# Performance work log

Hardware: AMD Instinct MI355X
Metric: run time of the kernel (lower is better)

The kernel has to match this reference:

```python
import jax, jax.numpy as jnp
import numpy as np

N, D, FF, NH = 500000, 128, 256, 4
GRIDS = [0.5, 1.0, 2.0]


def setup_inputs() -> dict:
    key = jax.random.key(0)
    ks = jax.random.split(key, 8)
    h = jax.random.normal(ks[0], (N, D), jnp.float32)
    coords = jax.random.uniform(ks[1], (N, 3), jnp.float32) * 8.0
    c = np.asarray(coords)
    invs, Ms = [], []
    for g in GRIDS:
        vox = np.floor(c / g).astype(np.int64)
        _, inv = np.unique(vox, axis=0, return_inverse=True)
        invs.append(jnp.asarray(inv.reshape(-1).astype(np.int32)))
        Ms.append(int(inv.max()) + 1)
    S = len(GRIDS)
    sc = 0.02
    def rn(k, shape):
        return jax.random.normal(k, shape, jnp.float32) * sc
    params = dict(
        Wqkv=rn(ks[2], (S, 3 * D, D)), bqkv=jnp.zeros((S, 3 * D), jnp.float32),
        Wo=rn(ks[3], (S, D, D)), bo=jnp.zeros((S, D), jnp.float32),
        ln1_s=jnp.ones((S, D), jnp.float32), ln1_b=jnp.zeros((S, D), jnp.float32),
        W1=rn(ks[4], (S, FF, D)), b1=jnp.zeros((S, FF), jnp.float32),
        W2=rn(ks[5], (S, D, FF)), b2=jnp.zeros((S, D), jnp.float32),
        ln2_s=jnp.ones((S, D), jnp.float32), ln2_b=jnp.zeros((S, D), jnp.float32),
        Wf=rn(ks[6], (D, D * (S + 1))), bf=jnp.zeros((D,), jnp.float32),
    )
    return dict(h=h, coords=coords, inv0=invs[0], inv1=invs[1], inv2=invs[2],
                M0=Ms[0], M1=Ms[1], M2=Ms[2], **params)


def _ln(x, s, b):
    m = x.mean(-1, keepdims=True)
    v = ((x - m) ** 2).mean(-1, keepdims=True)
    return (x - m) * jax.lax.rsqrt(v + 1e-5) * s + b


def _forward(h, invs, Ms, Wqkv, bqkv, Wo, bo, ln1_s, ln1_b, W1, b1, W2, b2, ln2_s, ln2_b, Wf, bf):
    dh = D // NH
    feats = [h]
    for i, (inv, M) in enumerate(zip(invs, Ms)):
        # scatter-mean pooling into M voxels (counts clamped >= 1)
        macro = jax.ops.segment_sum(h, inv, num_segments=M)  # [M, D]
        counts = jax.ops.segment_sum(jnp.ones((h.shape[0], 1), h.dtype), inv, num_segments=M)
        macro = macro / jnp.maximum(counts, 1.0)
        # TransformerEncoderLayer (post-norm, relu), batch of 1 -> drop batch dim
        qkv = macro @ Wqkv[i].T + bqkv[i]
        q, k, v = (t.reshape(M, NH, dh) for t in jnp.split(qkv, 3, axis=-1))
        scores = jnp.einsum('mhd,nhd->hmn', q, k) / jnp.sqrt(jnp.float32(dh))
        attn = jax.nn.softmax(scores, axis=-1)
        o = jnp.einsum('hmn,nhd->mhd', attn, v).reshape(M, D) @ Wo[i].T + bo[i]
        x = _ln(macro + o, ln1_s[i], ln1_b[i])
        ffo = jax.nn.relu(x @ W1[i].T + b1[i]) @ W2[i].T + b2[i]
        x = _ln(x + ffo, ln2_s[i], ln2_b[i])
        feats.append(x[inv])  # broadcast gather back to particles [N, D]
    return jnp.concatenate(feats, axis=-1) @ Wf.T + bf


def reference(h, coords, inv0, inv1, inv2, M0, M1, M2, Wqkv, bqkv, Wo, bo, ln1_s, ln1_b, W1, b1, W2, b2, ln2_s, ln2_b, Wf, bf):
    return _forward(h, (inv0, inv1, inv2), (M0, M1, M2), Wqkv, bqkv, Wo, bo,
                    ln1_s, ln1_b, W1, b1, W2, b2, ln2_s, ln2_b, Wf, bf)
```

## Files before the change

kernel.cpp:

```cpp
#include <hip/hip_runtime.h>
#include <hip/hip_bf16.h>

#define MC 4096
#define DD 128
#define NHH 4
#define DH 32
#define FFD 256
#define NS 3
#define NSPLIT 4
#define PLEN 1024

typedef __attribute__((ext_vector_type(8))) short short8_t;
typedef __attribute__((ext_vector_type(4))) float f32x4;

__device__ __forceinline__ int getM(int s, const int* M0, const int* M1, const int* M2) {
    return (s == 0) ? *M0 : (s == 1) ? *M1 : *M2;
}

__device__ __forceinline__ unsigned short f2bf(float f) {
    unsigned int u = __float_as_uint(f);
    u += 0x7FFFu + ((u >> 16) & 1u);
    return (unsigned short)(u >> 16);
}

__device__ __forceinline__ short8_t pack8(float4 a, float4 b) {
    short8_t r;
    r[0] = (short)f2bf(a.x); r[1] = (short)f2bf(a.y);
    r[2] = (short)f2bf(a.z); r[3] = (short)f2bf(a.w);
    r[4] = (short)f2bf(b.x); r[5] = (short)f2bf(b.y);
    r[6] = (short)f2bf(b.z); r[7] = (short)f2bf(b.w);
    return r;
}

__device__ __forceinline__ f32x4 max4(f32x4 a, f32x4 b) {
    f32x4 r;
    r[0] = fmaxf(a[0], b[0]); r[1] = fmaxf(a[1], b[1]);
    r[2] = fmaxf(a[2], b[2]); r[3] = fmaxf(a[3], b[3]);
    return r;
}
__device__ __forceinline__ f32x4 shflx4(f32x4 a, int m) {
    f32x4 r;
    r[0] = __shfl_xor(a[0], m); r[1] = __shfl_xor(a[1], m);
    r[2] = __shfl_xor(a[2], m); r[3] = __shfl_xor(a[3], m);
    return r;
}
__device__ __forceinline__ f32x4 exp4(f32x4 a) {
    f32x4 r;
    r[0] = __expf(a[0]); r[1] = __expf(a[1]);
    r[2] = __expf(a[2]); r[3] = __expf(a[3]);
    return r;
}

__global__ void k_parent(const int* __restrict__ inv0, const int* __restrict__ inv1,
                         const int* __restrict__ inv2,
                         int* __restrict__ parent10, int* __restrict__ parent21,
                         int* __restrict__ cnt, int N)
{
    int n = blockIdx.x * blockDim.x + threadIdx.x;
    if (n >= N) return;
    int i0 = inv0[n];
    parent10[i0] = inv1[n];
    parent21[inv1[n]] = inv2[n];
    atomicAdd(&cnt[i0], 1);
}

__global__ void k_scan(const int* __restrict__ cnt, int* __restrict__ offs)
{
    __shared__ int arr[1024];
    int tid = threadIdx.x;
    int base = tid * 4;
    int c0 = cnt[base], c1 = cnt[base + 1], c2 = cnt[base + 2], c3 = cnt[base + 3];
    int tot = c0 + c1 + c2 + c3;
    arr[tid] = tot;
    __syncthreads();
    for (int off = 1; off < 1024; off <<= 1) {
        int v = (tid >= off) ? arr[tid - off] : 0;
        __syncthreads();
        arr[tid] += v;
        __syncthreads();
    }
    int excl = arr[tid] - tot;
    offs[base] = excl;
    offs[base + 1] = excl + c0;
    offs[base + 2] = excl + c0 + c1;
    offs[base + 3] = excl + c0 + c1 + c2;
}

__global__ void k_place(const int* __restrict__ inv0, const int* __restrict__ offs,
                        int* __restrict__ fill, int* __restrict__ order, int N)
{
    int n = blockIdx.x * blockDim.x + threadIdx.x;
    if (n >= N) return;
    int i0 = inv0[n];
    int pos = offs[i0] + atomicAdd(&fill[i0], 1);
    order[pos] = n;
}

__global__ __launch_bounds__(256) void k_pool(const float* __restrict__ h,
                                              const int* __restrict__ order,
                                              const int* __restrict__ offs,
                                              const int* __restrict__ cnt,
                                              float* __restrict__ sum0, float* __restrict__ cnt0,
                                              const int* __restrict__ M0)
{
    int v = blockIdx.x;
    if (v >= *M0) return;
    int beg = offs[v], len = cnt[v];
    int tid = threadIdx.x;
    int dg = tid & 31;
    int rs = tid >> 5;
    const int* op = order + beg;

    float ax = 0.f, ay = 0.f, az = 0.f, aw = 0.f;
    int j = rs;
    for (; j + 8 < len; j += 16) {
        int r0 = op[j];
        int r1 = op[j + 8];
        float4 a = *(const float4*)(h + (size_t)r0 * DD + dg * 4);
        float4 b = *(const float4*)(h + (size_t)r1 * DD + dg * 4);
        ax += a.x + b.x; ay += a.y + b.y; az += a.z + b.z; aw += a.w + b.w;
    }
    if (j < len) {
        int r0 = op[j];
        float4 a = *(const float4*)(h + (size_t)r0 * DD + dg * 4);
        ax += a.x; ay += a.y; az += a.z; aw += a.w;
    }

    __shared__ __align__(16) float red[8][DD];
    *(float4*)&red[rs][dg * 4] = make_float4(ax, ay, az, aw);
    __syncthreads();
    if (tid < 32) {
        float4 t0 = *(const float4*)&red[0][tid * 4];
        float4 t1 = *(const float4*)&red[1][tid * 4];
        float4 t2 = *(const float4*)&red[2][tid * 4];
        float4 t3 = *(const float4*)&red[3][tid * 4];
        float4 t4 = *(const float4*)&red[4][tid * 4];
        float4 t5 = *(const float4*)&red[5][tid * 4];
        float4 t6 = *(const float4*)&red[6][tid * 4];
        float4 t7 = *(const float4*)&red[7][tid * 4];
        float4 r;
        r.x = ((t0.x + t1.x) + (t2.x + t3.x)) + ((t4.x + t5.x) + (t6.x + t7.x));
        r.y = ((t0.y + t1.y) + (t2.y + t3.y)) + ((t4.y + t5.y) + (t6.y + t7.y));
        r.z = ((t0.z + t1.z) + (t2.z + t3.z)) + ((t4.z + t5.z) + (t6.z + t7.z));
        r.w = ((t0.w + t1.w) + (t2.w + t3.w)) + ((t4.w + t5.w) + (t6.w + t7.w));
        *(float4*)(sum0 + (size_t)v * DD + tid * 4) = r;
        if (tid == 0) cnt0[v] = (float)len;
    }
}

__global__ void k_rollup(const float* __restrict__ sumSrc, const float* __restrict__ cntSrc,
                         const int* __restrict__ parent,
                         float* __restrict__ sumDst, float* __restrict__ cntDst,
                         const int* __restrict__ Msrc, int cap)
{
    int idx = blockIdx.x * blockDim.x + threadIdx.x;
    int v = idx >> 7, d = idx & 127;
    int Ms = *Msrc;
    if (Ms > cap) Ms = cap;
    if (v >= Ms) return;
    int p = parent[v];
    atomicAdd(&sumDst[(size_t)p * DD + d], sumSrc[idx]);
    if (d == 0) atomicAdd(&cntDst[p], cntSrc[v]);
}

__global__ void k_finalize(float* __restrict__ macro, const float* __restrict__ counts,
                           const int* M0, const int* M1, const int* M2)
{
    int idx = blockIdx.x * blockDim.x + threadIdx.x;
    int s = idx / (MC * DD);
    int r = (idx >> 7) & (MC - 1);
    if (r >= getM(s, M0, M1, M2)) return;
    float c = counts[s * MC + r];
    macro[idx] /= fmaxf(c, 1.0f);
}

__global__ void k_b0frag(const float* __restrict__ Wf, unsigned short* __restrict__ b0f)
{
    int idx = blockIdx.x * 256 + threadIdx.x;
    int j = idx & 7, l = (idx >> 3) & 63, kt = (idx >> 9) & 3, nt = idx >> 11;
    int d = nt * 16 + (l & 15);
    int k = kt * 32 + (l >> 4) * 8 + j;
    b0f[idx] = f2bf(Wf[(size_t)d * (4 * DD) + k]);
}

__global__ void k_qkv(const float* __restrict__ macro, const float* __restrict__ Wqkv,
                      const float* __restrict__ bqkv, float* __restrict__ qkv,
                      const int* M0, const int* M1, const int* M2)
{
    int s = blockIdx.y;
    int Ms = getM(s, M0, M1, M2);
    int row0 = blockIdx.x * 8;
    if (row0 >= Ms) return;
    __shared__ __align__(16) float mac[8][DD];
    int tid = threadIdx.x;
    for (int e = tid; e < 8 * DD; e += 256) {
        int r = e >> 7, d = e & 127;
        int row = row0 + r;
        mac[r][d] = (row < Ms) ? macro[(size_t)s * MC * DD + (size_t)row * DD + d] : 0.0f;
    }
    __syncthreads();
    for (int j = tid; j < 3 * DD; j += 256) {
        const float* w = Wqkv + ((size_t)s * 3 * DD + j) * DD;
        float b = bqkv[s * 3 * DD + j];
        float acc[8];
#pragma unroll
        for (int r = 0; r < 8; ++r) acc[r] = b;
        for (int k = 0; k < DD; k += 4) {
            float4 w4 = *(const float4*)(w + k);
#pragma unroll
            for (int r = 0; r < 8; ++r) {
                float4 m4 = *(const float4*)&mac[r][k];
                acc[r] += w4.x * m4.x + w4.y * m4.y + w4.z * m4.z + w4.w * m4.w;
            }
        }
        for (int r = 0; r < 8; ++r) {
            int row = row0 + r;
            if (row < Ms) qkv[((size_t)s * MC + row) * (3 * DD) + j] = acc[r];
        }
    }
}

__global__ __launch_bounds__(256) void k_attn_part(const float* __restrict__ qkv,
                                                   float* __restrict__ part_o,
                                                   float* __restrict__ part_ml,
                                                   const int* M0, const int* M1, const int* M2)
{
    int z = blockIdx.z;
    int s = z / NSPLIT, part = z % NSPLIT;
    int head = blockIdx.y;
    int Ms = getM(s, M0, M1, M2);
    int q0 = blockIdx.x * 64;
    if (q0 >= Ms) return;
    int kstart = part * PLEN;
    if (kstart >= Ms) return;
    int kend = kstart + PLEN; if (kend > Ms) kend = Ms;

    __shared__ __align__(16) unsigned short kf[4][64][8];
    __shared__ __align__(16) unsigned short vf[2][2][64][8];
    __shared__ __align__(16) unsigned short pf[4][16][80];

    int tid = threadIdx.x;
    int wave = tid >> 6, lane = tid & 63;
    int c = lane & 15, g = lane >> 4;

    const float* base = qkv + (size_t)s * MC * 3 * DD;
    const float* Qb = base + head * DH;
    const float* Kb = base + DD + head * DH;
    const float* Vb = base + 2 * DD + head * DH;

    short8_t qfrag = {0,0,0,0,0,0,0,0};
    {
        int qr = q0 + wave * 16 + c;
        if (qr < Ms) {
            const float* qp = Qb + (size_t)qr * 3 * DD + g * 8;
            qfrag = pack8(*(const float4*)qp, *(const float4*)(qp + 4));
        }
    }

    f32x4 o0 = {0.f, 0.f, 0.f, 0.f}, o1 = {0.f, 0.f, 0.f, 0.f};
    f32x4 mreg = {-1e30f, -1e30f, -1e30f, -1e30f};
    f32x4 lreg = {0.f, 0.f, 0.f, 0.f};
    const float scale = 0.1767766952966369f;

    int sko = tid >> 2, sg = tid & 3;
    int s_nt = sko >> 4;
    int s_l  = (sko & 15) | (sg << 4);
    int s_ks = sko >> 5, s_kk = sko & 31;
    int s_j  = s_kk & 7, s_hi = (s_kk >> 3) & 3;
    int s_vnt = sg >> 1, s_db = (sg & 1) * 8;

    for (int kb = kstart; kb < kend; kb += 64) {
        __syncthreads();
        {
            int key = kb + sko;
            short8_t kv = {0,0,0,0,0,0,0,0};
            if (key < kend) {
                const float* kr = Kb + (size_t)key * 3 * DD + sg * 8;
                kv = pack8(*(const float4*)kr, *(const float4*)(kr + 4));
            }
            *(short8_t*)&kf[s_nt][s_l][0] = kv;
        }
        {
            int key = kb + sko;
            float4 a = make_float4(0.f, 0.f, 0.f, 0.f);
            float4 b = make_float4(0.f, 0.f, 0.f, 0.f);
            if (key < kend) {
                const float* vr = Vb + (size_t)key * 3 * DD + sg * 8;
                a = *(const float4*)vr;
                b = *(const float4*)(vr + 4);
            }
            unsigned short* vslot = &vf[s_ks][s_vnt][0][0];
            vslot[((s_db + 0) | (s_hi << 4)) * 8 + s_j] = f2bf(a.x);
            vslot[((s_db + 1) | (s_hi << 4)) * 8 + s_j] = f2bf(a.y);
            vslot[((s_db + 2) | (s_hi << 4)) * 8 + s_j] = f2bf(a.z);
            vslot[((s_db + 3) | (s_hi << 4)) * 8 + s_j] = f2bf(a.w);
            vslot[((s_db + 4) | (s_hi << 4)) * 8 + s_j] = f2bf(b.x);
            vslot[((s_db + 5) | (s_hi << 4)) * 8 + s_j] = f2bf(b.y);
            vslot[((s_db + 6) | (s_hi << 4)) * 8 + s_j] = f2bf(b.z);
            vslot[((s_db + 7) | (s_hi << 4)) * 8 + s_j] = f2bf(b.w);
        }
        __syncthreads();

        f32x4 zero = {0.f, 0.f, 0.f, 0.f};
        short8_t kf0 = *(const short8_t*)&kf[0][lane][0];
        short8_t kf1 = *(const short8_t*)&kf[1][lane][0];
        short8_t kf2 = *(const short8_t*)&kf[2][lane][0];
        short8_t kf3 = *(const short8_t*)&kf[3][lane][0];
        f32x4 a0 = __builtin_amdgcn_mfma_f32_16x16x32_bf16(qfrag, kf0, zero, 0, 0, 0);
        f32x4 a1 = __builtin_amdgcn_mfma_f32_16x16x32_bf16(qfrag, kf1, zero, 0, 0, 0);
        f32x4 a2 = __builtin_amdgcn_mfma_f32_16x16x32_bf16(qfrag, kf2, zero, 0, 0, 0);
        f32x4 a3 = __builtin_amdgcn_mfma_f32_16x16x32_bf16(qfrag, kf3, zero, 0, 0, 0);

        f32x4 neg = {-1e30f, -1e30f, -1e30f, -1e30f};
        a0 = (kb +  0 + c < kend) ? a0 * scale : neg;
        a1 = (kb + 16 + c < kend) ? a1 * scale : neg;
        a2 = (kb + 32 + c < kend) ? a2 * scale : neg;
        a3 = (kb + 48 + c < kend) ? a3 * scale : neg;

        f32x4 rmax = max4(max4(a0, a1), max4(a2, a3));
        rmax = max4(rmax, shflx4(rmax, 1));
        rmax = max4(rmax, shflx4(rmax, 2));
        rmax = max4(rmax, shflx4(rmax, 4));
        rmax = max4(rmax, shflx4(rmax, 8));
        f32x4 mnew = max4(mreg, rmax);
        f32x4 alpha = exp4(mreg - mnew);
        mreg = mnew;
        lreg = lreg * alpha;
        o0 = o0 * alpha;
        o1 = o1 * alpha;

        a0 = exp4(a0 - mnew);
        a1 = exp4(a1 - mnew);
        a2 = exp4(a2 - mnew);
        a3 = exp4(a3 - mnew);
        f32x4 rsum = (a0 + a1) + (a2 + a3);
        rsum = rsum + shflx4(rsum, 1);
        rsum = rsum + shflx4(rsum, 2);
        rsum = rsum + shflx4(rsum, 4);
        rsum = rsum + shflx4(rsum, 8);
        lreg = lreg + rsum;

        {
            unsigned short* prow = &pf[wave][0][0];
            int rb = g * 4;
            prow[(rb + 0) * 80 +  0 + c] = f2bf(a0[0]);
            prow[(rb + 1) * 80 +  0 + c] = f2bf(a0[1]);
            prow[(rb + 2) * 80 +  0 + c] = f2bf(a0[2]);
            prow[(rb + 3) * 80 +  0 + c] = f2bf(a0[3]);
            prow[(rb + 0) * 80 + 16 + c] = f2bf(a1[0]);
            prow[(rb + 1) * 80 + 16 + c] = f2bf(a1[1]);
            prow[(rb + 2) * 80 + 16 + c] = f2bf(a1[2]);
            prow[(rb + 3) * 80 + 16 + c] = f2bf(a1[3]);
            prow[(rb + 0) * 80 + 32 + c] = f2bf(a2[0]);
            prow[(rb + 1) * 80 + 32 + c] = f2bf(a2[1]);
            prow[(rb + 2) * 80 + 32 + c] = f2bf(a2[2]);
            prow[(rb + 3) * 80 + 32 + c] = f2bf(a2[3]);
            prow[(rb + 0) * 80 + 48 + c] = f2bf(a3[0]);
            prow[(rb + 1) * 80 + 48 + c] = f2bf(a3[1]);
            prow[(rb + 2) * 80 + 48 + c] = f2bf(a3[2]);
            prow[(rb + 3) * 80 + 48 + c] = f2bf(a3[3]);
        }

        {
            short8_t p0 = *(const short8_t*)&pf[wave][c][ 0 + g * 8];
            short8_t v00 = *(const short8_t*)&vf[0][0][lane][0];
            short8_t v01 = *(const short8_t*)&vf[0][1][lane][0];
            o0 = __builtin_amdgcn_mfma_f32_16x16x32_bf16(p0, v00, o0, 0, 0, 0);
            o1 = __builtin_amdgcn_mfma_f32_16x16x32_bf16(p0, v01, o1, 0, 0, 0);
            short8_t p1 = *(const short8_t*)&pf[wave][c][32 + g * 8];
            short8_t v10 = *(const short8_t*)&vf[1][0][lane][0];
            short8_t v11 = *(const short8_t*)&vf[1][1][lane][0];
            o0 = __builtin_amdgcn_mfma_f32_16x16x32_bf16(p1, v10, o0, 0, 0, 0);
            o1 = __builtin_amdgcn_mfma_f32_16x16x32_bf16(p1, v11, o1, 0, 0, 0);
        }
    }

    int rec = ((s * NHH + head) * 64 + blockIdx.x) * NSPLIT + part;
    float* po = part_o + (size_t)rec * 2048;
    int qb = wave * 16 + g * 4;
    po[(qb + 0) * 32 + c] = o0[0];
    po[(qb + 1) * 32 + c] = o0[1];
    po[(qb + 2) * 32 + c] = o0[2];
    po[(qb + 3) * 32 + c] = o0[3];
    po[(qb + 0) * 32 + 16 + c] = o1[0];
    po[(qb + 1) * 32 + 16 + c] = o1[1];
    po[(qb + 2) * 32 + 16 + c] = o1[2];
    po[(qb + 3) * 32 + 16 + c] = o1[3];
    if (c == 0) {
        part_ml[rec * 128 + qb + 0] = mreg[0];
        part_ml[rec * 128 + qb + 1] = mreg[1];
        part_ml[rec * 128 + qb + 2] = mreg[2];
        part_ml[rec * 128 + qb + 3] = mreg[3];
        part_ml[rec * 128 + 64 + qb + 0] = lreg[0];
        part_ml[rec * 128 + 64 + qb + 1] = lreg[1];
        part_ml[rec * 128 + 64 + qb + 2] = lreg[2];
        part_ml[rec * 128 + 64 + qb + 3] = lreg[3];
    }
}

__global__ void k_attn_comb(const float* __restrict__ part_o, const float* __restrict__ part_ml,
                            float* __restrict__ attno,
                            const int* M0, const int* M1, const int* M2)
{
    int s = blockIdx.z, head = blockIdx.y;
    int Ms = getM(s, M0, M1, M2);
    int q0 = blockIdx.x * 64;
    if (q0 >= Ms) return;
    int tid = threadIdx.x;
    int qi = tid >> 2, sub = tid & 3;
    int nparts = (Ms + PLEN - 1) / PLEN;
    if (nparts > NSPLIT) nparts = NSPLIT;
    int recbase = ((s * NHH + head) * 64 + blockIdx.x) * NSPLIT;

    float m = -1e30f;
    for (int p = 0; p < nparts; ++p)
        m = fmaxf(m, part_ml[(recbase + p) * 128 + qi]);
    float L = 0.f;
    float4 A0 = {0,0,0,0}, A1 = {0,0,0,0};
    for (int p = 0; p < nparts; ++p) {
        float mp = part_ml[(recbase + p) * 128 + qi];
        float lp = part_ml[(recbase + p) * 128 + 64 + qi];
        float w = __expf(mp - m);
        L += lp * w;
        const float* po = part_o + (size_t)(recbase + p) * 2048;
        float4 a = *(const float4*)(po + qi * 32 + sub * 4);
        float4 b = *(const float4*)(po + qi * 32 + (sub + 4) * 4);
        A0.x += a.x * w; A0.y += a.y * w; A0.z += a.z * w; A0.w += a.w * w;
        A1.x += b.x * w; A1.y += b.y * w; A1.z += b.z * w; A1.w += b.w * w;
    }
    if (q0 + qi < Ms) {
        float inv = 1.0f / fmaxf(L, 1e-30f);
        size_t orow = ((size_t)s * MC + q0 + qi) * DD + head * DH;
        float4 r0 = make_float4(A0.x * inv, A0.y * inv, A0.z * inv, A0.w * inv);
        float4 r1 = make_float4(A1.x * inv, A1.y * inv, A1.z * inv, A1.w * inv);
        *(float4*)(attno + orow + sub * 4) = r0;
        *(float4*)(attno + orow + (sub + 4) * 4) = r1;
    }
}

__global__ __launch_bounds__(256) void k_layer(const float* __restrict__ macro,
                                               const float* __restrict__ attno,
                                               const float* __restrict__ Wo, const float* __restrict__ bo,
                                               const float* __restrict__ ln1s, const float* __restrict__ ln1b,
                                               const float* __restrict__ W1, const float* __restrict__ b1,
                                               const float* __restrict__ W2, const float* __restrict__ b2,
                                               const float* __restrict__ ln2s, const float* __restrict__ ln2b,
                                               const float* __restrict__ Wf,
                                               float* __restrict__ y,
                                               const int* M0, const int* M1, const int* M2)
{
    int s = blockIdx.y;
    int Ms = getM(s, M0, M1, M2);
    int row0 = blockIdx.x * 8;
    if (row0 >= Ms) return;
    __shared__ __align__(16) float os8[8][DD];
    __shared__ __align__(16) float xr8[8][DD];
    __shared__ __align__(16) float ts8[8][FFD];
    __shared__ float mv[8][2];
    int tid = threadIdx.x;
    int rr = tid >> 5, tt = tid & 31;

    {
        int row = row0 + rr;
        float4 v = make_float4(0.f, 0.f, 0.f, 0.f);
        if (row < Ms) v = *(const float4*)(attno + ((size_t)s * MC + row) * DD + tt * 4);
        *(float4*)&os8[rr][tt * 4] = v;
    }
    __syncthreads();

    float acc[8];

    if (tid < DD) {
        const float* w = Wo + ((size_t)s * DD + tid) * DD;
        float b = bo[s * DD + tid];
#pragma unroll
        for (int r = 0; r < 8; ++r) acc[r] = b;
        for (int k = 0; k < DD; k += 4) {
            float4 w4 = *(const float4*)(w + k);
#pragma unroll
            for (int r = 0; r < 8; ++r) {
                float4 m4 = *(const float4*)&os8[r][k];
                acc[r] += w4.x * m4.x + w4.y * m4.y + w4.z * m4.z + w4.w * m4.w;
            }
        }
#pragma unroll
        for (int r = 0; r < 8; ++r) {
            int row = row0 + r;
            float res = (row < Ms) ? macro[((size_t)s * MC + row) * DD + tid] : 0.f;
            xr8[r][tid] = acc[r] + res;
        }
    }
    __syncthreads();

    {
        float4 v = *(const float4*)&xr8[rr][tt * 4];
        float su = v.x + v.y + v.z + v.w;
        float sq = v.x * v.x + v.y * v.y + v.z * v.z + v.w * v.w;
        for (int off = 16; off >= 1; off >>= 1) { su += __shfl_xor(su, off); sq += __shfl_xor(sq, off); }
        if (tt == 0) { mv[rr][0] = su; mv[rr][1] = sq; }
    }
    __syncthreads();
    {
        float mean = mv[rr][0] * (1.0f / DD);
        float var = fmaxf(mv[rr][1] * (1.0f / DD) - mean * mean, 0.0f);
        float rstd = rsqrtf(var + 1e-5f);
        float4 v = *(const float4*)&xr8[rr][tt * 4];
        float4 gs = *(const float4*)(ln1s + s * DD + tt * 4);
        float4 gb = *(const float4*)(ln1b + s * DD + tt * 4);
        float4 o;
        o.x = (v.x - mean) * rstd * gs.x + gb.x;
        o.y = (v.y - mean) * rstd * gs.y + gb.y;
        o.z = (v.z - mean) * rstd * gs.z + gb.z;
        o.w = (v.w - mean) * rstd * gs.w + gb.w;
        *(float4*)&xr8[rr][tt * 4] = o;
    }
    __syncthreads();

    {
        const float* w = W1 + ((size_t)s * FFD + tid) * DD;
        float b = b1[s * FFD + tid];
#pragma unroll
        for (int r = 0; r < 8; ++r) acc[r] = b;
        for (int k = 0; k < DD; k += 4) {
            float4 w4 = *(const float4*)(w + k);
#pragma unroll
            for (int r = 0; r < 8; ++r) {
                float4 m4 = *(const float4*)&xr8[r][k];
                acc[r] += w4.x * m4.x + w4.y * m4.y + w4.z * m4.z + w4.w * m4.w;
            }
        }
#pragma unroll
        for (int r = 0; r < 8; ++r) ts8[r][tid] = fmaxf(acc[r], 0.0f);
    }
    __syncthreads();

    if (tid < DD) {
        const float* w = W2 + ((size_t)s * DD + tid) * FFD;
        float b = b2[s * DD + tid];
#pragma unroll
        for (int r = 0; r < 8; ++r) acc[r] = b;
        for (int k = 0; k < FFD; k += 4) {
            float4 w4 = *(const float4*)(w + k);
#pragma unroll
            for (int r = 0; r < 8; ++r) {
                float4 m4 = *(const float4*)&ts8[r][k];
                acc[r] += w4.x * m4.x + w4.y * m4.y + w4.z * m4.z + w4.w * m4.w;
            }
        }
#pragma unroll
        for (int r = 0; r < 8; ++r) os8[r][tid] = acc[r] + xr8[r][tid];
    }
    __syncthreads();

    {
        float4 v = *(const float4*)&os8[rr][tt * 4];
        float su = v.x + v.y + v.z + v.w;
        float sq = v.x * v.x + v.y * v.y + v.z * v.z + v.w * v.w;
        for (int off = 16; off >= 1; off >>= 1) { su += __shfl_xor(su, off); sq += __shfl_xor(sq, off); }
        if (tt == 0) { mv[rr][0] = su; mv[rr][1] = sq; }
    }
    __syncthreads();
    {
        float mean = mv[rr][0] * (1.0f / DD);
        float var = fmaxf(mv[rr][1] * (1.0f / DD) - mean * mean, 0.0f);
        float rstd = rsqrtf(var + 1e-5f);
        float4 v = *(const float4*)&os8[rr][tt * 4];
        float4 gs = *(const float4*)(ln2s + s * DD + tt * 4);
        float4 gb = *(const float4*)(ln2b + s * DD + tt * 4);
        float4 o;
        o.x = (v.x - mean) * rstd * gs.x + gb.x;
        o.y = (v.y - mean) * rstd * gs.y + gb.y;
        o.z = (v.z - mean) * rstd * gs.z + gb.z;
        o.w = (v.w - mean) * rstd * gs.w + gb.w;
        *(float4*)&os8[rr][tt * 4] = o;
    }
    __syncthreads();

    if (tid < DD) {
        const float* w = Wf + (size_t)tid * (4 * DD) + (s + 1) * DD;
#pragma unroll
        for (int r = 0; r < 8; ++r) acc[r] = 0.f;
        for (int k = 0; k < DD; k += 4) {
            float4 w4 = *(const float4*)(w + k);
#pragma unroll
            for (int r = 0; r < 8; ++r) {
                float4 m4 = *(const float4*)&os8[r][k];
                acc[r] += w4.x * m4.x + w4.y * m4.y + w4.z * m4.z + w4.w * m4.w;
            }
        }
#pragma unroll
        for (int r = 0; r < 8; ++r) {
            int row = row0 + r;
            if (row < Ms) y[((size_t)s * MC + row) * DD + tid] = acc[r];
        }
    }
}

__global__ void k_ycomb(const float* __restrict__ y, const int* __restrict__ parent10,
                        const int* __restrict__ parent21, const float* __restrict__ bf,
                        float* __restrict__ yc, const int* __restrict__ M0)
{
    int idx = blockIdx.x * 256 + threadIdx.x;
    int v = idx >> 7, d = idx & 127;
    if (v >= *M0) return;
    int p1 = parent10[v];
    int p2 = parent21[p1];
    yc[idx] = y[(size_t)v * DD + d] + y[((size_t)MC + p1) * DD + d]
            + y[((size_t)2 * MC + p2) * DD + d] + bf[d];
}

__global__ __launch_bounds__(256) void k_final(const float* __restrict__ h,
                                               const unsigned short* __restrict__ b0f,
                                               const float* __restrict__ yc,
                                               const int* __restrict__ inv0,
                                               float* __restrict__ out, int N)
{
    int tid = threadIdx.x;
    int wave = tid >> 6, lane = tid & 63;
    int c = lane & 15, g = lane >> 4;

    int ntasks = (N + 15) >> 4;
    int pair = blockIdx.x * 4 + wave;
    int taskA = pair * 2;
    if (taskA >= ntasks) return;
    int taskB = taskA + 1;

    int pA = taskA * 16 + c;
    int pB = taskB * 16 + c;
    bool okA = (pA < N);
    bool okB = (taskB < ntasks) && (pB < N);

    short8_t hA0 = {0,0,0,0,0,0,0,0}, hA1 = hA0, hA2 = hA0, hA3 = hA0;
    short8_t hB0 = hA0, hB1 = hA0, hB2 = hA0, hB3 = hA0;
    int iA = 0, iB = 0;
    if (okA) {
        const float* hr = h + (size_t)pA * DD + g * 8;
        hA0 = pack8(*(const float4*)(hr +  0), *(const float4*)(hr +  4));
        hA1 = pack8(*(const float4*)(hr + 32), *(const float4*)(hr + 36));
        hA2 = pack8(*(const float4*)(hr + 64), *(const float4*)(hr + 68));
        hA3 = pack8(*(const float4*)(hr + 96), *(const float4*)(hr + 100));
        iA = inv0[pA];
    }
    if (okB) {
        const float* hr = h + (size_t)pB * DD + g * 8;
        hB0 = pack8(*(const float4*)(hr +  0), *(const float4*)(hr +  4));
        hB1 = pack8(*(const float4*)(hr + 32), *(const float4*)(hr + 36));
        hB2 = pack8(*(const float4*)(hr + 64), *(const float4*)(hr + 68));
        hB3 = pack8(*(const float4*)(hr + 96), *(const float4*)(hr + 100));
        iB = inv0[pB];
    }
    const float* ycA = yc + (size_t)iA * DD;
    const float* ycB = yc + (size_t)iB * DD;

#pragma unroll
    for (int ntp = 0; ntp < 4; ++ntp) {
        int nt0 = ntp * 2, nt1 = ntp * 2 + 1;
        f32x4 aA0 = {0.f, 0.f, 0.f, 0.f}, aA1 = {0.f, 0.f, 0.f, 0.f};
        f32x4 aB0 = {0.f, 0.f, 0.f, 0.f}, aB1 = {0.f, 0.f, 0.f, 0.f};
        {
            short8_t w00 = *(const short8_t*)(b0f + (size_t)((nt0 * 4 + 0) * 64 + lane) * 8);
            aA0 = __builtin_amdgcn_mfma_f32_16x16x32_bf16(w00, hA0, aA0, 0, 0, 0);
            aB0 = __builtin_amdgcn_mfma_f32_16x16x32_bf16(w00, hB0, aB0, 0, 0, 0);
            short8_t w10 = *(const short8_t*)(b0f + (size_t)((nt1 * 4 + 0) * 64 + lane) * 8);
            aA1 = __builtin_amdgcn_mfma_f32_16x16x32_bf16(w10, hA0, aA1, 0, 0, 0);
            aB1 = __builtin_amdgcn_mfma_f32_16x16x32_bf16(w10, hB0, aB1, 0, 0, 0);
            short8_t w01 = *(const short8_t*)(b0f + (size_t)((nt0 * 4 + 1) * 64 + lane) * 8);
            aA0 = __builtin_amdgcn_mfma_f32_16x16x32_bf16(w01, hA1, aA0, 0, 0, 0);
            aB0 = __builtin_amdgcn_mfma_f32_16x16x32_bf16(w01, hB1, aB0, 0, 0, 0);
            short8_t w11 = *(const short8_t*)(b0f + (size_t)((nt1 * 4 + 1) * 64 + lane) * 8);
            aA1 = __builtin_amdgcn_mfma_f32_16x16x32_bf16(w11, hA1, aA1, 0, 0, 0);
            aB1 = __builtin_amdgcn_mfma_f32_16x16x32_bf16(w11, hB1, aB1, 0, 0, 0);
            short8_t w02 = *(const short8_t*)(b0f + (size_t)((nt0 * 4 + 2) * 64 + lane) * 8);
            aA0 = __builtin_amdgcn_mfma_f32_16x16x32_bf16(w02, hA2, aA0, 0, 0, 0);
            aB0 = __builtin_amdgcn_mfma_f32_16x16x32_bf16(w02, hB2, aB0, 0, 0, 0);
            short8_t w12 = *(const short8_t*)(b0f + (size_t)((nt1 * 4 + 2) * 64 + lane) * 8);
            aA1 = __builtin_amdgcn_mfma_f32_16x16x32_bf16(w12, hA2, aA1, 0, 0, 0);
            aB1 = __builtin_amdgcn_mfma_f32_16x16x32_bf16(w12, hB2, aB1, 0, 0, 0);
            short8_t w03 = *(const short8_t*)(b0f + (size_t)((nt0 * 4 + 3) * 64 + lane) * 8);
            aA0 = __builtin_amdgcn_mfma_f32_16x16x32_bf16(w03, hA3, aA0, 0, 0, 0);
            aB0 = __builtin_amdgcn_mfma_f32_16x16x32_bf16(w03, hB3, aB0, 0, 0, 0);
            short8_t w13 = *(const short8_t*)(b0f + (size_t)((nt1 * 4 + 3) * 64 + lane) * 8);
            aA1 = __builtin_amdgcn_mfma_f32_16x16x32_bf16(w13, hA3, aA1, 0, 0, 0);
            aB1 = __builtin_amdgcn_mfma_f32_16x16x32_bf16(w13, hB3, aB1, 0, 0, 0);
        }
        int d0 = nt0 * 16 + g * 4;
        int d1 = d0 + 16;
        if (okA) {
            float4 g0 = *(const float4*)(ycA + d0);
            float4 g1 = *(const float4*)(ycA + d1);
            float4 r0, r1;
            r0.x = aA0[0] + g0.x; r0.y = aA0[1] + g0.y; r0.z = aA0[2] + g0.z; r0.w = aA0[3] + g0.w;
            r1.x = aA1[0] + g1.x; r1.y = aA1[1] + g1.y; r1.z = aA1[2] + g1.z; r1.w = aA1[3] + g1.w;
            *(float4*)(out + (size_t)pA * DD + d0) = r0;
            *(float4*)(out + (size_t)pA * DD + d1) = r1;
        }
        if (okB) {
            float4 g0 = *(const float4*)(ycB + d0);
            float4 g1 = *(const float4*)(ycB + d1);
            float4 r0, r1;
            r0.x = aB0[0] + g0.x; r0.y = aB0[1] + g0.y; r0.z = aB0[2] + g0.z; r0.w = aB0[3] + g0.w;
            r1.x = aB1[0] + g1.x; r1.y = aB1[1] + g1.y; r1.z = aB1[2] + g1.z; r1.w = aB1[3] + g1.w;
            *(float4*)(out + (size_t)pB * DD + d0) = r0;
            *(float4*)(out + (size_t)pB * DD + d1) = r1;
        }
    }
}

extern "C" void kernel_launch(void* const* d_in, const int* in_sizes, int n_in,
                              void* d_out, int out_size, void* d_ws, size_t ws_size,
                              hipStream_t stream) {
    (void)n_in; (void)out_size; (void)ws_size;
    const float* h   = (const float*)d_in[0];
    const int* inv0  = (const int*)d_in[2];
    const int* inv1  = (const int*)d_in[3];
    const int* inv2  = (const int*)d_in[4];
    const int* M0    = (const int*)d_in[5];
    const int* M1    = (const int*)d_in[6];
    const int* M2    = (const int*)d_in[7];
    const float* Wqkv = (const float*)d_in[8];
    const float* bqkv = (const float*)d_in[9];
    const float* Wo   = (const float*)d_in[10];
    const float* bo   = (const float*)d_in[11];
    const float* ln1s = (const float*)d_in[12];
    const float* ln1b = (const float*)d_in[13];
    const float* W1   = (const float*)d_in[14];
    const float* b1   = (const float*)d_in[15];
    const float* W2   = (const float*)d_in[16];
    const float* b2   = (const float*)d_in[17];
    const float* ln2s = (const float*)d_in[18];
    const float* ln2b = (const float*)d_in[19];
    const float* Wf   = (const float*)d_in[20];
    const float* bf   = (const float*)d_in[21];
    int N = in_sizes[0] / DD;

    float* ws      = (float*)d_ws;
    float* macro   = ws;
    float* counts  = macro + (size_t)NS * MC * DD;
    float* qkvb    = counts + (size_t)NS * MC;
    float* attno   = qkvb + (size_t)NS * MC * 3 * DD;
    float* yb      = attno + (size_t)NS * MC * DD;
    float* b0f_f   = yb + (size_t)NS * MC * DD;
    unsigned short* b0f = (unsigned short*)b0f_f;
    float* part_o  = b0f_f + (size_t)DD * DD;
    float* part_ml = part_o + (size_t)NS * NHH * 64 * NSPLIT * 2048;
    float* ycb     = part_ml + (size_t)NS * NHH * 64 * NSPLIT * 128;
    int* ip        = (int*)(ycb + (size_t)MC * DD);
    int* parent10  = ip;
    int* parent21  = parent10 + MC;
    int* cnt_i     = parent21 + 512;
    int* fill      = cnt_i + MC;
    int* offs      = fill + MC;
    int* order     = offs + MC;

    float* sum0 = macro;
    float* sum1 = macro + (size_t)1 * MC * DD;
    float* sum2 = macro + (size_t)2 * MC * DD;
    float* cnt0 = counts;
    float* cnt1 = counts + MC;
    float* cnt2 = counts + 2 * MC;

    hipMemsetAsync(macro, 0, ((size_t)NS * MC * DD + NS * MC) * sizeof(float), stream);
    hipMemsetAsync(cnt_i, 0, (size_t)2 * MC * sizeof(int), stream);

    int nb = (N + 255) / 256;
    k_parent<<<nb, 256, 0, stream>>>(inv0, inv1, inv2, parent10, parent21, cnt_i, N);
    k_scan<<<1, 1024, 0, stream>>>(cnt_i, offs);
    k_place<<<nb, 256, 0, stream>>>(inv0, offs, fill, order, N);
    k_pool<<<MC, 256, 0, stream>>>(h, order, offs, cnt_i, sum0, cnt0, M0);
    k_rollup<<<(MC * DD) / 256, 256, 0, stream>>>(sum0, cnt0, parent10, sum1, cnt1, M0, MC);
    k_rollup<<<(512 * DD) / 256, 256, 0, stream>>>(sum1, cnt1, parent21, sum2, cnt2, M1, 512);
    k_finalize<<<(NS * MC * DD) / 256, 256, 0, stream>>>(macro, counts, M0, M1, M2);
    k_b0frag<<<64, 256, 0, stream>>>(Wf, b0f);
    k_qkv<<<dim3(MC / 8, NS), 256, 0, stream>>>(macro, Wqkv, bqkv, qkvb, M0, M1, M2);
    k_attn_part<<<dim3(MC / 64, NHH, NS * NSPLIT), 256, 0, stream>>>(qkvb, part_o, part_ml, M0, M1, M2);
    k_attn_comb<<<dim3(MC / 64, NHH, NS), 256, 0, stream>>>(part_o, part_ml, attno, M0, M1, M2);
    k_layer<<<dim3(MC / 8, NS), 256, 0, stream>>>(macro, attno, Wo, bo, ln1s, ln1b,
                                                  W1, b1, W2, b2, ln2s, ln2b, Wf, yb, M0, M1, M2);
    k_ycomb<<<(MC * DD) / 256, 256, 0, stream>>>(yb, parent10, parent21, bf, ycb, M0);
    int ntasks = (N + 15) >> 4;
    int npairs = (ntasks + 1) / 2;
    k_final<<<(npairs + 3) / 4, 256, 0, stream>>>(h, b0f, ycb, inv0, (float*)d_out, N);
}
```

Measured before the change: 461.4 us.

## Double-buffer K/V tiles in LDS for split attention kernel

Splits the K and V shared-memory tiles into two buffers and stages the next 64-key block while the current one is consumed, with one barrier per iteration instead of two. The goal is to overlap global loads and bf16 conversion with the MFMA and softmax work and to remove a sync. It doubles LDS use for K/V and raises register pressure, which may lower occupancy. Attention is only one of several kernels in the pipeline.

Result: no change. 460.4 us, median of 2 (-0.2%).

```diff
diff --git a/kernel.cpp b/kernel.cpp
--- a/kernel.cpp
+++ b/kernel.cpp
@@ -235,8 +235,8 @@
     if (kstart >= Ms) return;
     int kend = kstart + PLEN; if (kend > Ms) kend = Ms;
 
-    __shared__ __align__(16) unsigned short kf[4][64][8];
-    __shared__ __align__(16) unsigned short vf[2][2][64][8];
+    __shared__ __align__(16) unsigned short kf[2][4][64][8];
+    __shared__ __align__(16) unsigned short vf[2][2][2][64][8];
     __shared__ __align__(16) unsigned short pf[4][16][80];
 
     int tid = threadIdx.x;
@@ -269,8 +269,7 @@
     int s_j  = s_kk & 7, s_hi = (s_kk >> 3) & 3;
     int s_vnt = sg >> 1, s_db = (sg & 1) * 8;
 
-    for (int kb = kstart; kb < kend; kb += 64) {
-        __syncthreads();
+    auto STAGE = [&](int buf, int kb) {
         {
             int key = kb + sko;
             short8_t kv = {0,0,0,0,0,0,0,0};
@@ -278,7 +277,7 @@
                 const float* kr = Kb + (size_t)key * 3 * DD + sg * 8;
                 kv = pack8(*(const float4*)kr, *(const float4*)(kr + 4));
             }
-            *(short8_t*)&kf[s_nt][s_l][0] = kv;
+            *(short8_t*)&kf[buf][s_nt][s_l][0] = kv;
         }
         {
             int key = kb + sko;
@@ -289,7 +288,7 @@
                 a = *(const float4*)vr;
                 b = *(const float4*)(vr + 4);
             }
-            unsigned short* vslot = &vf[s_ks][s_vnt][0][0];
+            unsigned short* vslot = &vf[buf][s_ks][s_vnt][0][0];
             vslot[((s_db + 0) | (s_hi << 4)) * 8 + s_j] = f2bf(a.x);
             vslot[((s_db + 1) | (s_hi << 4)) * 8 + s_j] = f2bf(a.y);
             vslot[((s_db + 2) | (s_hi << 4)) * 8 + s_j] = f2bf(a.z);
@@ -299,13 +298,20 @@
             vslot[((s_db + 6) | (s_hi << 4)) * 8 + s_j] = f2bf(b.z);
             vslot[((s_db + 7) | (s_hi << 4)) * 8 + s_j] = f2bf(b.w);
         }
-        __syncthreads();
+    };
+
+    STAGE(0, kstart);
+    __syncthreads();
+    int cur = 0;
+
+    for (int kb = kstart; kb < kend; kb += 64) {
+        if (kb + 64 < kend) STAGE(cur ^ 1, kb + 64);
 
         f32x4 zero = {0.f, 0.f, 0.f, 0.f};
-        short8_t kf0 = *(const short8_t*)&kf[0][lane][0];
-        short8_t kf1 = *(const short8_t*)&kf[1][lane][0];
-        short8_t kf2 = *(const short8_t*)&kf[2][lane][0];
-        short8_t kf3 = *(const short8_t*)&kf[3][lane][0];
+        short8_t kf0 = *(const short8_t*)&kf[cur][0][lane][0];
+        short8_t kf1 = *(const short8_t*)&kf[cur][1][lane][0];
+        short8_t kf2 = *(const short8_t*)&kf[cur][2][lane][0];
+        short8_t kf3 = *(const short8_t*)&kf[cur][3][lane][0];
         f32x4 a0 = __builtin_amdgcn_mfma_f32_16x16x32_bf16(qfrag, kf0, zero, 0, 0, 0);
         f32x4 a1 = __builtin_amdgcn_mfma_f32_16x16x32_bf16(qfrag, kf1, zero, 0, 0, 0);
         f32x4 a2 = __builtin_amdgcn_mfma_f32_16x16x32_bf16(qfrag, kf2, zero, 0, 0, 0);
@@ -363,16 +369,19 @@
 
         {
             short8_t p0 = *(const short8_t*)&pf[wave][c][ 0 + g * 8];
-            short8_t v00 = *(const short8_t*)&vf[0][0][lane][0];
-            short8_t v01 = *(const short8_t*)&vf[0][1][lane][0];
+            short8_t v00 = *(const short8_t*)&vf[cur][0][0][lane][0];
+            short8_t v01 = *(const short8_t*)&vf[cur][0][1][lane][0];
             o0 = __builtin_amdgcn_mfma_f32_16x16x32_bf16(p0, v00, o0, 0, 0, 0);
             o1 = __builtin_amdgcn_mfma_f32_16x16x32_bf16(p0, v01, o1, 0, 0, 0);
             short8_t p1 = *(const short8_t*)&pf[wave][c][32 + g * 8];
-            short8_t v10 = *(const short8_t*)&vf[1][0][lane][0];
-            short8_t v11 = *(const short8_t*)&vf[1][1][lane][0];
+            short8_t v10 = *(const short8_t*)&vf[cur][1][0][lane][0];
+            short8_t v11 = *(const short8_t*)&vf[cur][1][1][lane][0];
             o0 = __builtin_amdgcn_mfma_f32_16x16x32_bf16(p1, v10, o0, 0, 0, 0);
             o1 = __builtin_amdgcn_mfma_f32_16x16x32_bf16(p1, v11, o1, 0, 0, 0);
         }
+
+        __syncthreads();
+        cur ^= 1;
     }
 
     int rec = ((s * NHH + head) * 64 + blockIdx.x) * NSPLIT + part;
```
